# Kernel tuning notes

Hardware: AMD Instinct MI355X
Metric: run time of the kernel (lower is better)

Reference implementation:

```python
import jax, jax.numpy as jnp
import numpy as np

N_ATOMS = 128
BATCH = 512


def _build_buffers(n):
    # Segments: all non-adjacent bond pairs (i,i+1,j,j+1), j >= i+2, j+1 <= n-1.
    segs = np.array([(i, i + 1, j, j + 1)
                     for i in range(n - 3)
                     for j in range(i + 2, n - 1)], dtype=np.int32)  # (S,4)

    def pidx(a, b):  # linear index of pair (a,b), a<b, in row-major triu(offset=1) order
        return a * n - a * (a + 1) // 2 + (b - a - 1)

    # Each writhe value scatters into its 4 incident residue pairs.
    # Pairs (0,1) [triu idx 0] and (n-2,n-1) [last triu idx] are never incident,
    # so ranks among interior pairs are (triu idx - 1); they are re-inserted by pad.
    inc = []
    for (i, _, j, _) in segs:
        for (a, b) in ((i, j), (i, j + 1), (i + 1, j), (i + 1, j + 1)):
            inc.append(pidx(a, b) - 1)
    indices = np.array(inc, dtype=np.int32)  # (4*S,)

    # Sort permutation placing [upper-triu values, lower-triu values] into
    # row-major order of all off-diagonal (r,c) entries, keyed by r*n + c.
    iu = np.stack(np.triu_indices(n, 1))  # (2, P) row-major
    vals = np.concatenate([iu[0] * n + iu[1], iu[1] * n + iu[0]])
    sort = np.argsort(vals).astype(np.int32)  # (n^2 - n,)
    return segs, indices, sort


def setup_inputs() -> dict:
    key = jax.random.key(0)
    xyz = jax.random.normal(key, (BATCH, N_ATOMS, 3), dtype=jnp.float32)
    segs, indices, sort = _build_buffers(N_ATOMS)
    return {
        "xyz": xyz,
        "segments": jnp.asarray(segs),
        "indices": jnp.asarray(indices),
        "sort": jnp.asarray(sort),
    }


def _divnorm(x):
    return x / jnp.linalg.norm(x, axis=-1, keepdims=True)


def _writhe(xyz, segments):
    # xyz: (B,N,3); segments: (S,4) -> writhe per segment pair, (B,S)
    B, S = xyz.shape[0], segments.shape[0]
    p = xyz[:, segments]  # (B,S,4,3) gathered endpoints [s1a,s1b,s2a,s2b]
    # d[k] = normalize(p_{2+j} - p_i), k = 2*i + j  (the 4 inter-segment directions)
    d = _divnorm((p[:, :, None, 2:, :] - p[:, :, :2, None, :]).reshape(B, S, 4, 3))
    axial = jnp.cross(p[:, :, 3] - p[:, :, 2], p[:, :, 1] - p[:, :, 0])  # (B,S,3)
    signs = jnp.sign(jnp.sum(axial * d[:, :, 0], -1))  # (B,S)
    # 4 face normals of the spherical quadrilateral, then Gauss-Bonnet angle sum
    nrm = _divnorm(jnp.cross(d[:, :, jnp.array([0, 1, 3, 2])],
                             d[:, :, jnp.array([1, 3, 2, 0])]))  # (B,S,4,3)
    cosang = jnp.clip(jnp.sum(nrm * nrm[:, :, jnp.array([1, 2, 3, 0])], -1), -1.0, 1.0)
    omega = jnp.arcsin(cosang).sum(-1)  # (B,S)
    return omega * signs / (2.0 * jnp.pi)


def _laplacian(wr, indices, sort, n):
    # wr: (B,S); scatter-add each writhe into its 4 incident residue pairs,
    # pad back the two untouched pairs, symmetrize, and sort into row-major
    # off-diagonal order -> (B, n^2 - n)
    M = (n * n - n) // 2 - 2
    triu = jnp.zeros((wr.shape[0], M), wr.dtype).at[:, indices].add(
        jnp.repeat(wr, 4, axis=1))
    padded = jnp.pad(triu, ((0, 0), (1, 1)))
    return jnp.concatenate([padded, padded], axis=1)[:, sort]


def reference(xyz, segments, indices, sort):
    xyz = xyz.reshape(-1, N_ATOMS, 3)
    wr = _writhe(xyz, segments)
    return _laplacian(wr, indices, sort, N_ATOMS)
```

## Files before the change

### kernel.cpp

```cpp
#include <hip/hip_runtime.h>
#include <math.h>

#define NATOMS    128
#define NSEG      7875
#define M_TRIU    8126
#define PADLEN    8128
#define OUT_PER_B 16256
#define BLOCK     1024

struct F3 { float x, y, z; };
__device__ __forceinline__ F3 f3sub(F3 a, F3 b) { return {a.x - b.x, a.y - b.y, a.z - b.z}; }
__device__ __forceinline__ F3 f3cross(F3 a, F3 b) {
    return {a.y * b.z - a.z * b.y, a.z * b.x - a.x * b.z, a.x * b.y - a.y * b.x};
}
__device__ __forceinline__ float f3dot(F3 a, F3 b) { return a.x * b.x + a.y * b.y + a.z * b.z; }
__device__ __forceinline__ float clip1(float x) { return fminf(1.0f, fmaxf(-1.0f, x)); }

__device__ __forceinline__ float fast_asin(float x) {
    float a = fabsf(x);
    float p = -0.0187293f;
    p = fmaf(p, a,  0.0742610f);
    p = fmaf(p, a, -0.2121144f);
    p = fmaf(p, a,  1.5707288f);
    float r = 1.57079632679f - __builtin_amdgcn_sqrtf(1.0f - a) * p;
    return copysignf(r, x);
}

__device__ __forceinline__ int seg_row_base(int i) { return 125 * i - (__umul24(i, i - 1) >> 1); }
__device__ __forceinline__ int pair_row_base(int a) { return (__umul24(a, 255 - a) >> 1); }

__device__ __forceinline__ float seg_writhe_packed(unsigned pack, const float* sx,
                                                   const float* sy, const float* sz) {
    int j = (int)(pack & 127u);
    int i = (int)(pack >> 7);

    F3 p0 = {sx[i],     sy[i],     sz[i]};
    F3 p1 = {sx[i + 1], sy[i + 1], sz[i + 1]};
    F3 p2 = {sx[j],     sy[j],     sz[j]};
    F3 p3 = {sx[j + 1], sy[j + 1], sz[j + 1]};

    F3 u0 = f3sub(p2, p0);
    F3 u1 = f3sub(p3, p0);
    F3 u2 = f3sub(p2, p1);
    F3 u3 = f3sub(p3, p1);

    F3 n0 = f3cross(u0, u1);
    F3 n1 = f3cross(u1, u3);
    F3 n2 = f3cross(u3, u2);
    F3 n3 = f3cross(u2, u0);

    F3 axial = f3cross(f3sub(u3, u2), f3sub(u0, u2));
    float sd = f3dot(axial, u0);
    float sgn = (sd > 0.0f) ? 1.0f : ((sd < 0.0f) ? -1.0f : 0.0f);

    float q0 = f3dot(n0, n0);
    float q1 = f3dot(n1, n1);
    float q2 = f3dot(n2, n2);
    float q3 = f3dot(n3, n3);

    float c0 = clip1(f3dot(n0, n1) * __builtin_amdgcn_rsqf(q0 * q1));
    float c1 = clip1(f3dot(n1, n2) * __builtin_amdgcn_rsqf(q1 * q2));
    float c2 = clip1(f3dot(n2, n3) * __builtin_amdgcn_rsqf(q2 * q3));
    float c3 = clip1(f3dot(n3, n0) * __builtin_amdgcn_rsqf(q3 * q0));

    float omega = fast_asin(c0) + fast_asin(c1) + fast_asin(c2) + fast_asin(c3);
    return omega * sgn * 0.15915494309189535f;
}

__global__ __launch_bounds__(BLOCK, 8) void writhe_fused(
    const float* __restrict__ xyz,
    float*       __restrict__ out)
{
    __shared__ float sx[NATOMS], sy[NATOMS], sz[NATOMS];
    __shared__ float swr[NSEG];
    __shared__ float triu[M_TRIU];
    unsigned short* sidx = (unsigned short*)triu;

    const int b = blockIdx.x;
    const int t = threadIdx.x;

    if (t < 3 * NATOMS) {
        float v = xyz[(size_t)b * (3 * NATOMS) + t];
        int a = t / 3, c = t - 3 * a;
        if (c == 0) sx[a] = v; else if (c == 1) sy[a] = v; else sz[a] = v;
    }

    {
        int s = t * 8;
        if (s < NSEG) {
            int i = (int)((251.0f - __builtin_amdgcn_sqrtf(63001.0f - 8.0f * (float)s)) * 0.5f);
            i = max(i, 0);
            i += (seg_row_base(i + 1) <= s);
            i += (seg_row_base(i + 1) <= s);
            i -= (seg_row_base(i) > s);
            i -= (seg_row_base(i) > s);
            int j = s - seg_row_base(i) + i + 2;
            #pragma unroll
            for (int k = 0; k < 8; ++k) {
                if (s < NSEG) sidx[s] = (unsigned short)((i << 7) | j);
                ++s; ++j;
                if (j > 126) { ++i; j = i + 2; }
            }
        }
    }
    __syncthreads();

    #pragma unroll
    for (int half = 0; half < 2; ++half) {
        const int s0 = half * 4096 + t;
        unsigned pk[4];
        bool     vl[4];
        #pragma unroll
        for (int k = 0; k < 4; ++k) {
            int s = s0 + k * 1024;
            vl[k] = (s < NSEG);
            pk[k] = sidx[vl[k] ? s : (NSEG - 1)];
        }
        float w[4];
        #pragma unroll
        for (int k = 0; k < 4; ++k)
            w[k] = seg_writhe_packed(pk[k], sx, sy, sz);
        #pragma unroll
        for (int k = 0; k < 4; ++k)
            if (vl[k]) swr[s0 + k * 1024] = w[k];
    }
    __syncthreads();

    for (int m = t; m < M_TRIU; m += BLOCK) {
        int q = m + 1;
        int a = (int)((255.0f - __builtin_amdgcn_sqrtf(65025.0f - 8.0f * (float)q)) * 0.5f);
        a = max(a, 0);
        a += (pair_row_base(a + 1) <= q);
        a += (pair_row_base(a + 1) <= q);
        a -= (pair_row_base(a) > q);
        a -= (pair_row_base(a) > q);
        int bb = a + 1 + (q - pair_row_base(a));

        float sum = 0.0f;
        #pragma unroll
        for (int di = -1; di <= 0; ++di) {
            #pragma unroll
            for (int dj = -1; dj <= 0; ++dj) {
                int i = a + di, j = bb + dj;
                bool valid = (i >= 0) && (i <= 124) && (j >= i + 2) && (j <= 126);
                int s = valid ? (seg_row_base(i) + (j - i - 2)) : 0;
                float v = swr[s];
                sum += valid ? v : 0.0f;
            }
        }
        triu[m] = sum;
    }
    __syncthreads();

    float* ob = out + (size_t)b * OUT_PER_B;
    for (int k = t; k < OUT_PER_B; k += BLOCK) {
        unsigned r  = (unsigned)k / 127u;
        unsigned cc = (unsigned)k - 127u * r;
        unsigned c  = cc + (cc >= r);
        int a  = (int)min(r, c);
        int bb = (int)max(r, c);
        int p  = pair_row_base(a) + bb - a - 1;
        float val = (p == 0 || p == PADLEN - 1) ? 0.0f : triu[p - 1];
        ob[k] = val;
    }
}

extern "C" void kernel_launch(void* const* d_in, const int* in_sizes, int n_in,
                              void* d_out, int out_size, void* d_ws, size_t ws_size,
                              hipStream_t stream) {
    const float* xyz = (const float*)d_in[0];
    float*       out = (float*)d_out;

    int B = in_sizes[0] / (NATOMS * 3);
    writhe_fused<<<B, BLOCK, 0, stream>>>(xyz, out);
}
```

Before: 96.60 us.

## Fuse pair summation with symmetric output writes using precomputed pair table

Replaces the separate triu-accumulation and output-gather passes with one loop over pairs that sums the four incident writhe values and stores to both symmetric output positions. Pair coordinates come from a packed LDS table built alongside the segment table, which removes the per-element sqrt/division index recovery. This drops one barrier and the intermediate triu buffer. The transposed store is strided, so global write coalescing gets worse.

```diff
diff --git a/kernel.cpp b/kernel.cpp
--- a/kernel.cpp
+++ b/kernel.cpp
@@ -3,8 +3,7 @@
 
 #define NATOMS    128
 #define NSEG      7875
-#define M_TRIU    8126
-#define PADLEN    8128
+#define NPAIR     8128
 #define OUT_PER_B 16256
 #define BLOCK     1024
 
@@ -73,8 +72,8 @@
 {
     __shared__ float sx[NATOMS], sy[NATOMS], sz[NATOMS];
     __shared__ float swr[NSEG];
-    __shared__ float triu[M_TRIU];
-    unsigned short* sidx = (unsigned short*)triu;
+    __shared__ unsigned short sidx[NSEG];
+    __shared__ unsigned short spair[NPAIR];
 
     const int b = blockIdx.x;
     const int t = threadIdx.x;
@@ -103,6 +102,24 @@
             }
         }
     }
+    {
+        int p = t * 8;
+        if (p < NPAIR) {
+            int a = (int)((255.0f - __builtin_amdgcn_sqrtf(65025.0f - 8.0f * (float)p)) * 0.5f);
+            a = max(a, 0);
+            a += (pair_row_base(a + 1) <= p);
+            a += (pair_row_base(a + 1) <= p);
+            a -= (pair_row_base(a) > p);
+            a -= (pair_row_base(a) > p);
+            int bb = a + 1 + (p - pair_row_base(a));
+            #pragma unroll
+            for (int k = 0; k < 8; ++k) {
+                if (p < NPAIR) spair[p] = (unsigned short)((a << 7) | bb);
+                ++p; ++bb;
+                if (bb > 127) { ++a; bb = a + 1; }
+            }
+        }
+    }
     __syncthreads();
 
     #pragma unroll
@@ -126,42 +143,33 @@
     }
     __syncthreads();
 
-    for (int m = t; m < M_TRIU; m += BLOCK) {
-        int q = m + 1;
-        int a = (int)((255.0f - __builtin_amdgcn_sqrtf(65025.0f - 8.0f * (float)q)) * 0.5f);
-        a = max(a, 0);
-        a += (pair_row_base(a + 1) <= q);
-        a += (pair_row_base(a + 1) <= q);
-        a -= (pair_row_base(a) > q);
-        a -= (pair_row_base(a) > q);
-        int bb = a + 1 + (q - pair_row_base(a));
+    float* ob = out + (size_t)b * OUT_PER_B;
+    for (int p = t; p < NPAIR; p += BLOCK) {
+        unsigned pk = spair[p];
+        int bb = (int)(pk & 127u);
+        int a  = (int)(pk >> 7);
 
-        float sum = 0.0f;
-        #pragma unroll
-        for (int di = -1; di <= 0; ++di) {
-            #pragma unroll
-            for (int dj = -1; dj <= 0; ++dj) {
-                int i = a + di, j = bb + dj;
-                bool valid = (i >= 0) && (i <= 124) && (j >= i + 2) && (j <= 126);
-                int s = valid ? (seg_row_base(i) + (j - i - 2)) : 0;
-                float v = swr[s];
-                sum += valid ? v : 0.0f;
-            }
-        }
-        triu[m] = sum;
-    }
-    __syncthreads();
+        int am1 = a - 1;
+        int s00 = 125 * am1 - ((am1 * (am1 - 1)) >> 1) + bb - a - 2;
+        int s10 = s00 + 125 - a;
 
-    float* ob = out + (size_t)b * OUT_PER_B;
-    for (int k = t; k < OUT_PER_B; k += BLOCK) {
-        unsigned r  = (unsigned)k / 127u;
-        unsigned cc = (unsigned)k - 127u * r;
-        unsigned c  = cc + (cc >= r);
-        int a  = (int)min(r, c);
-        int bb = (int)max(r, c);
-        int p  = pair_row_base(a) + bb - a - 1;
-        float val = (p == 0 || p == PADLEN - 1) ? 0.0f : triu[p - 1];
-        ob[k] = val;
+        bool v00 = (a >= 1) && (a <= 125) && (bb >= a + 2);
+        bool v01 = (a >= 1) && (a <= 125) && (bb <= 126);
+        bool v10 = (a <= 124) && (bb >= a + 3);
+        bool v11 = (a <= 124) && (bb <= 126) && (bb >= a + 2);
+
+        int c00 = min(max(s00,     0), NSEG - 1);
+        int c01 = min(max(s00 + 1, 0), NSEG - 1);
+        int c10 = min(max(s10,     0), NSEG - 1);
+        int c11 = min(max(s10 + 1, 0), NSEG - 1);
+
+        float sum = (v00 ? swr[c00] : 0.0f) + (v01 ? swr[c01] : 0.0f)
+                  + (v10 ? swr[c10] : 0.0f) + (v11 ? swr[c11] : 0.0f);
+
+        int k1 = 127 * a + bb - 1;
+        int k2 = 127 * bb + a;
+        ob[k1] = sum;
+        ob[k2] = sum;
     }
 }
 
```

Result: no change. 95.73 us (-0.9%).
